# Kernel tuning notes

Hardware: AMD Instinct MI355X
Metric: run time of the kernel (lower is better)

The kernel has to match this reference:

```python
import jax, jax.numpy as jnp
import numpy as np

N, E, C, L, G, O = 100000, 1600000, 128, 7, 2, 40
BETA = 0.9
HEADS, HC = 1, 128  # heads=1, head_channels=hidden_channels=128


def setup_inputs() -> dict:
    key = jax.random.key(0)
    ks = jax.random.split(key, 16)
    s = 0.05  # ~ torch Linear init std for fan_in=128
    inp = {
        'x': jax.random.normal(ks[0], (N, C), jnp.float32),
        'edge_index': jax.random.randint(ks[1], (2, E), 0, N, jnp.int64),
        'Wh': jax.random.normal(ks[2], (L, C, C)) * s,
        'bh': jax.random.normal(ks[3], (L, C)) * s,
        'Wg': jax.random.normal(ks[4], (L, C, C)) * s,
        'bg': jax.random.normal(ks[5], (L, C)) * s,
        'Wl': jax.random.normal(ks[6], (L, C, C)) * s,
        'bl': jax.random.normal(ks[7], (L, C)) * s,
        'ln_g': jnp.ones((L, C)), 'ln_b': jnp.zeros((L, C)),
        'bn_g': jnp.ones((L, C)), 'bn_b': jnp.zeros((L, C)),
        'bn_rm': jnp.zeros((L, C)), 'bn_rv': jnp.ones((L, C)),
        'gWh': jax.random.normal(ks[8], (G, C, C)) * s,
        'gbh': jax.random.normal(ks[9], (G, C)) * s,
        'gWk': jax.random.normal(ks[10], (G, C, C)) * s,
        'gWv': jax.random.normal(ks[11], (G, C, C)) * s,
        'gln_g': jnp.ones((G, C)), 'gln_b': jnp.zeros((G, C)),
        'gWo': jax.random.normal(ks[12], (G, C, C)) * s,
        'gbo': jax.random.normal(ks[13], (G, C)) * s,
        'f_ln_g': jnp.ones((C,)), 'f_ln_b': jnp.zeros((C,)),
        'Wp': jax.random.normal(ks[14], (O, C)) * s,
        'bp': jax.random.normal(ks[15], (O,)) * s,
    }
    return inp


def _layer_norm(x, g, b, eps=1e-5):
    mu = jnp.mean(x, axis=-1, keepdims=True)
    var = jnp.mean((x - mu) ** 2, axis=-1, keepdims=True)
    return (x - mu) * jax.lax.rsqrt(var + eps) * g + b


def reference(x, edge_index, Wh, bh, Wg, bg, Wl, bl, ln_g, ln_b,
              bn_g, bn_b, bn_rm, bn_rv, gWh, gbh, gWk, gWv,
              gln_g, gln_b, gWo, gbo, f_ln_g, f_ln_b, Wp, bp):
    n = x.shape[0]
    src, dst = edge_index[0], edge_index[1]
    # gcn_norm with add_self_loops=True: deg over destination incl. self loop
    deg = jnp.zeros((n,), x.dtype).at[dst].add(1.0) + 1.0
    dinv = jax.lax.rsqrt(deg)
    enorm = (dinv[src] * dinv[dst])[:, None]   # [E,1]
    selfw = (dinv * dinv)[:, None]             # [N,1] self-loop weight

    x_local = jnp.zeros_like(x @ Wh[0].T)
    for i in range(L):
        h = jax.nn.relu(x @ Wh[i].T + bh[i])
        xw = x @ Wg[i].T                                  # GCN lin (bias separate)
        agg = jax.ops.segment_sum(xw[src] * enorm, dst, num_segments=n)
        conv = agg + xw * selfw + bg[i]
        x = conv + x @ Wl[i].T + bl[i]
        # BatchNorm1d in eval mode (running stats)
        x = (x - bn_rm[i]) * jax.lax.rsqrt(bn_rv[i] + 1e-5) * bn_g[i] + bn_b[i]
        x = jax.nn.relu(x)
        x = (1.0 - BETA) * _layer_norm(h * x, ln_g[i], ln_b[i]) + BETA * x
        x_local = x_local + x

    # global linear attention (PolynormerAttention, qk_shared=True, qkv_bias=False)
    xg = _layer_norm(x_local, f_ln_g, f_ln_b)
    for j in range(G):
        h = xg @ gWh[j].T + gbh[j]
        k = jax.nn.sigmoid(xg @ gWk[j].T).reshape(n, HEADS, HC)
        q = k
        v = (xg @ gWv[j].T).reshape(n, HEADS, HC)
        kv = jnp.einsum('ndh,ndm->dhm', k, v)            # [heads,hc,hc]
        num = jnp.einsum('ndh,dhm->ndm', q, kv)          # [N,heads,hc]
        k_sum = jnp.sum(k, axis=0)                       # [heads,hc]
        den = jnp.einsum('ndh,dh->nd', q, k_sum)[..., None]
        attn = (num / (den + 1e-6)).reshape(n, HEADS * HC)
        xg = _layer_norm(attn, gln_g[j], gln_b[j]) * (h + BETA)
        xg = jax.nn.relu(xg @ gWo[j].T + gbo[j])

    return xg @ Wp.T + bp
```

## Files before the change

### kernel.cpp

```cpp
#include <hip/hip_runtime.h>

typedef unsigned short u16;
typedef unsigned int u32;
typedef __attribute__((ext_vector_type(8))) short short8;
typedef __attribute__((ext_vector_type(8))) unsigned short ushort8v;
typedef __attribute__((ext_vector_type(4))) float f32x4;

#define CDIM 128

__device__ __forceinline__ float b2f(u16 u){ return __uint_as_float(((unsigned)u)<<16); }
__device__ __forceinline__ u16 f2b(float f){
  unsigned x = __float_as_uint(f);
  unsigned r = (x + 0x7fffu + ((x>>16)&1u)) >> 16;
  return (u16)r;
}
__device__ __forceinline__ float wsum64(float v){
  #pragma unroll
  for(int d=1; d<64; d<<=1) v += __shfl_xor(v, d, 64);
  return v;
}
__device__ __forceinline__ float wsum16(float v){
  v += __shfl_xor(v, 1, 64);
  v += __shfl_xor(v, 2, 64);
  v += __shfl_xor(v, 4, 64);
  v += __shfl_xor(v, 8, 64);
  return v;
}

__global__ void k_probe(const u32* __restrict__ x, const u32* __restrict__ ei, int* __restrict__ flags){
  __shared__ int s_bf, s_nz;
  if(threadIdx.x == 0){ s_bf = 0; s_nz = 0; }
  __syncthreads();
  int c_bf = 0, c_nz = 0;
  for(int i = threadIdx.x; i < 4096; i += 256){
    u32 w = x[i];
    u32 e = (w >> 7) & 0xFFu;
    if(e >= 100u && e <= 140u) c_bf++;
    if(ei[2*i + 1] != 0u) c_nz++;
  }
  atomicAdd(&s_bf, c_bf);
  atomicAdd(&s_nz, c_nz);
  __syncthreads();
  if(threadIdx.x == 0){
    flags[0] = (s_bf < 2048) ? 1 : 0;
    flags[1] = (s_nz < 8) ? 1 : 0;
  }
}

__global__ void k_cvt_x(const void* __restrict__ src, u16* __restrict__ dst, int n,
                        const int* __restrict__ flags){
  int i = (blockIdx.x*256 + threadIdx.x)*8;
  if(i + 7 >= n) return;
  if(flags[0]){
    const float* s = (const float*)src + i;
    float4 a = *(const float4*)s;
    float4 b = *(const float4*)(s + 4);
    ushort8v o;
    o[0]=f2b(a.x); o[1]=f2b(a.y); o[2]=f2b(a.z); o[3]=f2b(a.w);
    o[4]=f2b(b.x); o[5]=f2b(b.y); o[6]=f2b(b.z); o[7]=f2b(b.w);
    *(ushort8v*)(dst + i) = o;
  } else {
    *(ushort8v*)(dst + i) = *(const ushort8v*)((const u16*)src + i);
  }
}

struct CvtArgs {
  const void* src[24];
  u16* dst[24];
  int n[24];
};

__global__ void k_cvt_params(CvtArgs a, const int* __restrict__ flags){
  int seg = blockIdx.y;
  int i = blockIdx.x*256 + threadIdx.x;
  int n = a.n[seg];
  if(i >= n) return;
  if(flags[0]) a.dst[seg][i] = f2b(((const float*)a.src[seg])[i]);
  else         a.dst[seg][i] = ((const u16*)a.src[seg])[i];
}

__global__ void k_cvt_ei_count(const int* __restrict__ src, int* __restrict__ dst, int E,
                               const int* __restrict__ flags, u32* __restrict__ cnt){
  int i = blockIdx.x*256 + threadIdx.x;
  if(i >= 2*E) return;
  int v = flags[1] ? src[2*i] : src[i];
  dst[i] = v;
  if(i >= E) atomicAdd(&cnt[v], 1u);
}

__global__ __launch_bounds__(256) void k_scan1(const u32* __restrict__ cnt, int n, u32* __restrict__ bsum){
  const int lane = threadIdx.x & 63;
  const int wv = threadIdx.x >> 6;
  int i = blockIdx.x*256 + threadIdx.x;
  u32 v = (i < n) ? cnt[i] : 0u;
  #pragma unroll
  for(int d=1; d<64; d<<=1) v += (u32)__shfl_xor((int)v, d, 64);
  __shared__ u32 ws[4];
  if(lane == 0) ws[wv] = v;
  __syncthreads();
  if(threadIdx.x == 0) bsum[blockIdx.x] = ws[0] + ws[1] + ws[2] + ws[3];
}

__global__ __launch_bounds__(1024) void k_scan2(const u32* __restrict__ bsum, int nb, u32* __restrict__ bpre){
  __shared__ u32 s[1024];
  int t = threadIdx.x;
  u32 v = (t < nb) ? bsum[t] : 0u;
  s[t] = v;
  __syncthreads();
  for(int d=1; d<1024; d<<=1){
    u32 y = (t >= d) ? s[t-d] : 0u;
    __syncthreads();
    s[t] += y;
    __syncthreads();
  }
  if(t < nb) bpre[t] = s[t] - v;
}

__global__ __launch_bounds__(256) void k_scan3(const u32* __restrict__ cnt, int n,
                                               const u32* __restrict__ bpre,
                                               u32* __restrict__ rowstart, u32* __restrict__ cursor,
                                               float* __restrict__ dinv){
  const int lane = threadIdx.x & 63;
  const int wv = threadIdx.x >> 6;
  int i = blockIdx.x*256 + threadIdx.x;
  u32 v = (i < n) ? cnt[i] : 0u;
  u32 x = v;
  #pragma unroll
  for(int d=1; d<64; d<<=1){
    u32 y = (u32)__shfl_up((int)x, d, 64);
    if(lane >= d) x += y;
  }
  __shared__ u32 ws[4];
  if(lane == 63) ws[wv] = x;
  __syncthreads();
  u32 woff = 0;
  #pragma unroll
  for(int w=0; w<4; w++) if(w < wv) woff += ws[w];
  u32 incl = x + woff;
  u32 rs = bpre[blockIdx.x] + incl - v;
  if(i < n){
    rowstart[i] = rs;
    cursor[i] = rs;
    dinv[i] = rsqrtf((float)(v + 1u));
    if(i == n-1) rowstart[n] = rs + v;
  }
}

__global__ void k_scatter(const int* __restrict__ ei, int E, u32* __restrict__ cursor,
                          const float* __restrict__ dinv, int2* __restrict__ colw){
  int e = blockIdx.x*256 + threadIdx.x;
  if(e < E){
    int s = ei[e];
    u32 p = atomicAdd(&cursor[ei[E + e]], 1u);
    colw[p] = make_int2(s, __float_as_int(dinv[s]));
  }
}

__global__ __launch_bounds__(256) void k_gemm3(
  const u16* __restrict__ A, int M,
  const u16* __restrict__ W0, const u16* __restrict__ bs0, int op0, u16* __restrict__ O0,
  const u16* __restrict__ W1, const u16* __restrict__ bs1, int op1, u16* __restrict__ O1,
  const u16* __restrict__ W2, const u16* __restrict__ bs2, int op2, u16* __restrict__ O2)
{
  const int lane = threadIdx.x & 63;
  const int wv = threadIdx.x >> 6;
  const int l16 = lane & 15, quad = lane >> 4;
  const long rbase = (long)blockIdx.x*128 + wv*32;

  short8 af[2][4];
  #pragma unroll
  for(int rt=0; rt<2; rt++){
    long r = rbase + rt*16 + l16; if(r >= M) r = M-1;
    const u16* ap = A + r*CDIM + quad*8;
    #pragma unroll
    for(int kt=0; kt<4; kt++)
      af[rt][kt] = *(const short8*)(ap + kt*32);
  }

  const u16* Ws[3] = {W0, W1, W2};
  const u16* Bs[3] = {bs0, bs1, bs2};
  u16* Os[3] = {O0, O1, O2};
  const int ops[3] = {op0, op1, op2};

  for(int w=0; w<3; w++){
    const u16* Wm = Ws[w];
    if(!Wm) break;
    const int op = ops[w];
    u16* Op = Os[w];
    const u16* bp = Bs[w];
    for(int ct=0; ct<8; ct++){
      f32x4 acc0 = {0.f,0.f,0.f,0.f}, acc1 = {0.f,0.f,0.f,0.f};
      const u16* wp = Wm + (ct*16 + l16)*CDIM + quad*8;
      #pragma unroll
      for(int kt=0; kt<4; kt++){
        short8 bf = *(const short8*)(wp + kt*32);
        acc0 = __builtin_amdgcn_mfma_f32_16x16x32_bf16(af[0][kt], bf, acc0, 0, 0, 0);
        acc1 = __builtin_amdgcn_mfma_f32_16x16x32_bf16(af[1][kt], bf, acc1, 0, 0, 0);
      }
      const int col = ct*16 + l16;
      const float bias = bp ? b2f(bp[col]) : 0.f;
      #pragma unroll
      for(int rt=0; rt<2; rt++){
        f32x4 a = rt ? acc1 : acc0;
        #pragma unroll
        for(int g=0; g<4; g++){
          long r = rbase + rt*16 + quad*4 + g;
          if(r < M){
            float v = a[g] + bias;
            if(op == 1) v = fmaxf(v, 0.f);
            else if(op == 2) v = 1.f/(1.f + __expf(-v));
            Op[r*CDIM + col] = f2b(v);
          }
        }
      }
    }
  }
}

__global__ __launch_bounds__(256) void k_layer_epi(
  const u16* __restrict__ xw, const u16* __restrict__ h, const u16* __restrict__ xl,
  const int2* __restrict__ colw, const u32* __restrict__ rowstart, const float* __restrict__ dinv,
  const u16* __restrict__ bg, const u16* __restrict__ bng, const u16* __restrict__ bnb,
  const u16* __restrict__ bnrm, const u16* __restrict__ bnrv,
  const u16* __restrict__ lng, const u16* __restrict__ lnb,
  float* __restrict__ xlocal, u16* __restrict__ xout, int n, int first)
{
  const int lane = threadIdx.x & 63;
  const int node = blockIdx.x*4 + (threadIdx.x >> 6);
  if(node >= n) return;
  const int c0 = lane*2;
  u32 j0 = rowstart[node], j1 = rowstart[node+1];
  float a0 = 0.f, a1 = 0.f;
  for(u32 base = j0; base < j1; base += 64){
    int avail = (int)(j1 - base);
    int cnt = avail < 64 ? avail : 64;
    int2 pw = make_int2(0, 0);
    if(lane < cnt) pw = colw[base + lane];
    int t = 0;
    for(; t + 8 <= cnt; t += 8){
      int s[8]; float w[8]; ushort2 v[8];
      #pragma unroll
      for(int k2=0;k2<8;k2++){
        s[k2] = __shfl(pw.x, t+k2, 64);
        w[k2] = __int_as_float(__shfl(pw.y, t+k2, 64));
      }
      #pragma unroll
      for(int k2=0;k2<8;k2++) v[k2] = *(const ushort2*)(xw + (size_t)s[k2]*CDIM + c0);
      #pragma unroll
      for(int k2=0;k2<8;k2++){
        a0 = fmaf(w[k2], b2f(v[k2].x), a0);
        a1 = fmaf(w[k2], b2f(v[k2].y), a1);
      }
    }
    for(; t + 2 <= cnt; t += 2){
      int s0 = __shfl(pw.x, t, 64),   s1 = __shfl(pw.x, t+1, 64);
      float w0 = __int_as_float(__shfl(pw.y, t, 64));
      float w1 = __int_as_float(__shfl(pw.y, t+1, 64));
      ushort2 v0 = *(const ushort2*)(xw + (size_t)s0*CDIM + c0);
      ushort2 v1 = *(const ushort2*)(xw + (size_t)s1*CDIM + c0);
      a0 = fmaf(w0, b2f(v0.x), a0); a1 = fmaf(w0, b2f(v0.y), a1);
      a0 = fmaf(w1, b2f(v1.x), a0); a1 = fmaf(w1, b2f(v1.y), a1);
    }
    for(; t < cnt; t++){
      int s0 = __shfl(pw.x, t, 64);
      float w0 = __int_as_float(__shfl(pw.y, t, 64));
      ushort2 vv = *(const ushort2*)(xw + (size_t)s0*CDIM + c0);
      a0 = fmaf(w0, b2f(vv.x), a0);
      a1 = fmaf(w0, b2f(vv.y), a1);
    }
  }
  float dn = dinv[node], sw = dn*dn;
  size_t base = (size_t)node*CDIM + c0;
  ushort2 xwv = *(const ushort2*)(xw + base);
  ushort2 xlv = *(const ushort2*)(xl + base);
  ushort2 hv  = *(const ushort2*)(h  + base);
  float x10 = a0*dn + b2f(xwv.x)*sw + b2f(bg[c0])   + b2f(xlv.x);
  float x11 = a1*dn + b2f(xwv.y)*sw + b2f(bg[c0+1]) + b2f(xlv.y);
  float s0 = rsqrtf(b2f(bnrv[c0])   + 1e-5f) * b2f(bng[c0]);
  float s1 = rsqrtf(b2f(bnrv[c0+1]) + 1e-5f) * b2f(bng[c0+1]);
  float x20 = (x10 - b2f(bnrm[c0]))*s0   + b2f(bnb[c0]);
  float x21 = (x11 - b2f(bnrm[c0+1]))*s1 + b2f(bnb[c0+1]);
  float x30 = fmaxf(x20, 0.f);
  float x31 = fmaxf(x21, 0.f);
  float t0 = b2f(hv.x)*x30, t1 = b2f(hv.y)*x31;
  float mu = wsum64(t0 + t1) * (1.f/128.f);
  float d0 = t0 - mu, d1 = t1 - mu;
  float var = wsum64(d0*d0 + d1*d1) * (1.f/128.f);
  float inv = rsqrtf(var + 1e-5f);
  float y0 = d0*inv*b2f(lng[c0])   + b2f(lnb[c0]);
  float y1 = d1*inv*b2f(lng[c0+1]) + b2f(lnb[c0+1]);
  float xn0 = 0.1f*y0 + 0.9f*x30;
  float xn1 = 0.1f*y1 + 0.9f*x31;
  float2 xl2;
  if(first){
    xl2.x = xn0; xl2.y = xn1;
  } else {
    xl2 = *(float2*)(xlocal + base);
    xl2.x += xn0; xl2.y += xn1;
  }
  *(float2*)(xlocal + base) = xl2;
  ushort2 o; o.x = f2b(xn0); o.y = f2b(xn1);
  *(ushort2*)(xout + base) = o;
}

__global__ __launch_bounds__(256) void k_ln(
  const float* __restrict__ xin, const u16* __restrict__ g, const u16* __restrict__ b,
  u16* __restrict__ out, int n)
{
  const int lane = threadIdx.x & 63;
  const int node = blockIdx.x*4 + (threadIdx.x >> 6);
  if(node >= n) return;
  const int c0 = lane*2;
  size_t base = (size_t)node*CDIM + c0;
  float2 v = *(const float2*)(xin + base);
  float mu = wsum64(v.x + v.y) * (1.f/128.f);
  float d0 = v.x - mu, d1 = v.y - mu;
  float var = wsum64(d0*d0 + d1*d1) * (1.f/128.f);
  float inv = rsqrtf(var + 1e-5f);
  ushort2 o;
  o.x = f2b(d0*inv*b2f(g[c0])   + b2f(b[c0]));
  o.y = f2b(d1*inv*b2f(g[c0+1]) + b2f(b[c0+1]));
  *(ushort2*)(out + base) = o;
}

__global__ __launch_bounds__(256) void k_kv(
  const u16* __restrict__ kk, const u16* __restrict__ vv, int n, int npb,
  float* __restrict__ part)
{
  __shared__ float sk[8][128];
  __shared__ float sv[8][128];
  const int tid = threadIdx.x;
  const int tr = tid >> 4, tc = tid & 15;
  float acc[8][8];
  #pragma unroll
  for(int i=0;i<8;i++){
    #pragma unroll
    for(int j=0;j<8;j++) acc[i][j] = 0.f;
  }
  float ks[8];
  #pragma unroll
  for(int i=0;i<8;i++) ks[i] = 0.f;
  int start = blockIdx.x * npb;
  int end = start + npb; if(end > n) end = n;
  const int lr = tid >> 5;
  const int lc = (tid & 31) * 4;
  for(int g0 = start; g0 < end; g0 += 8){
    int cnt = end - g0; if(cnt > 8) cnt = 8;
    __syncthreads();
    if(lr < cnt){
      ushort4 kq = *(const ushort4*)(kk + (size_t)(g0+lr)*CDIM + lc);
      ushort4 vq = *(const ushort4*)(vv + (size_t)(g0+lr)*CDIM + lc);
      sk[lr][lc] = b2f(kq.x); sk[lr][lc+1] = b2f(kq.y); sk[lr][lc+2] = b2f(kq.z); sk[lr][lc+3] = b2f(kq.w);
      sv[lr][lc] = b2f(vq.x); sv[lr][lc+1] = b2f(vq.y); sv[lr][lc+2] = b2f(vq.z); sv[lr][lc+3] = b2f(vq.w);
    }
    __syncthreads();
    for(int r=0; r<cnt; r++){
      float4 ka = *(const float4*)&sk[r][tr*8];
      float4 kb = *(const float4*)&sk[r][tr*8+4];
      float4 va = *(const float4*)&sv[r][tc*8];
      float4 vb = *(const float4*)&sv[r][tc*8+4];
      float kr[8] = {ka.x,ka.y,ka.z,ka.w,kb.x,kb.y,kb.z,kb.w};
      float vr[8] = {va.x,va.y,va.z,va.w,vb.x,vb.y,vb.z,vb.w};
      #pragma unroll
      for(int i=0;i<8;i++){
        #pragma unroll
        for(int j=0;j<8;j++) acc[i][j] = fmaf(kr[i], vr[j], acc[i][j]);
      }
      if(tc == 0){
        #pragma unroll
        for(int i=0;i<8;i++) ks[i] += kr[i];
      }
    }
  }
  float* p = part + (size_t)blockIdx.x * 16512;
  #pragma unroll
  for(int i=0;i<8;i++){
    #pragma unroll
    for(int j=0;j<8;j++)
      p[(size_t)(tc*8+j)*CDIM + tr*8 + i] = acc[i][j];
  }
  if(tc == 0){
    #pragma unroll
    for(int i=0;i<8;i++) p[16384 + tr*8 + i] = ks[i];
  }
}

__global__ void k_kvred(const float* __restrict__ part, int nb, u16* __restrict__ Bext){
  int i = blockIdx.x*256 + threadIdx.x;
  if(i >= 144*128) return;
  float s = 0.f;
  if(i < 16512){
    #pragma unroll 8
    for(int b=0;b<nb;b++) s += part[(size_t)b*16512 + i];
  }
  Bext[i] = f2b(s);
}

__global__ __launch_bounds__(256) void k_attn(
  const u16* __restrict__ q, const u16* __restrict__ Bext, const u16* __restrict__ hg,
  const u16* __restrict__ g, const u16* __restrict__ b,
  u16* __restrict__ out, int M)
{
  const int lane = threadIdx.x & 63;
  const int wv = threadIdx.x >> 6;
  const int l16 = lane & 15, quad = lane >> 4;
  const long rbase = (long)blockIdx.x*128 + wv*32;

  short8 af[2][4];
  #pragma unroll
  for(int rt=0; rt<2; rt++){
    long r = rbase + rt*16 + l16; if(r >= M) r = M-1;
    const u16* ap = q + r*CDIM + quad*8;
    #pragma unroll
    for(int kt=0; kt<4; kt++)
      af[rt][kt] = *(const short8*)(ap + kt*32);
  }
  f32x4 acc[2][9];
  f32x4 zero = {0.f,0.f,0.f,0.f};
  #pragma unroll
  for(int rt=0; rt<2; rt++){
    #pragma unroll
    for(int ct=0; ct<9; ct++) acc[rt][ct] = zero;
  }
  #pragma unroll
  for(int ct=0; ct<9; ct++){
    const u16* wp = Bext + (ct*16 + l16)*CDIM + quad*8;
    #pragma unroll
    for(int kt=0; kt<4; kt++){
      short8 bf = *(const short8*)(wp + kt*32);
      acc[0][ct] = __builtin_amdgcn_mfma_f32_16x16x32_bf16(af[0][kt], bf, acc[0][ct], 0, 0, 0);
      acc[1][ct] = __builtin_amdgcn_mfma_f32_16x16x32_bf16(af[1][kt], bf, acc[1][ct], 0, 0, 0);
    }
  }
  #pragma unroll
  for(int rt=0; rt<2; rt++){
    float rden[4];
    #pragma unroll
    for(int gi=0; gi<4; gi++){
      float dv = __shfl(acc[rt][8][gi], lane & 48, 64);
      rden[gi] = 1.f/(dv + 1e-6f);
    }
    #pragma unroll
    for(int gi=0; gi<4; gi++){
      float sum = 0.f;
      #pragma unroll
      for(int ct=0; ct<8; ct++) sum += acc[rt][ct][gi]*rden[gi];
      float mu = wsum16(sum) * (1.f/128.f);
      float vs = 0.f;
      #pragma unroll
      for(int ct=0; ct<8; ct++){ float d = acc[rt][ct][gi]*rden[gi] - mu; vs = fmaf(d, d, vs); }
      float inv = rsqrtf(wsum16(vs)*(1.f/128.f) + 1e-5f);
      long r = rbase + rt*16 + quad*4 + gi;
      if(r < M){
        #pragma unroll
        for(int ct=0; ct<8; ct++){
          int col = ct*16 + l16;
          float y = (acc[rt][ct][gi]*rden[gi] - mu)*inv*b2f(g[col]) + b2f(b[col]);
          float hvv = b2f(hg[(size_t)r*CDIM + col]);
          out[(size_t)r*CDIM + col] = f2b(y*(hvv + 0.9f));
        }
      }
    }
  }
}

__global__ __launch_bounds__(256) void k_gout(
  const u16* __restrict__ A, const u16* __restrict__ W, const u16* __restrict__ bs,
  void* __restrict__ outv, int M, const int* __restrict__ flags)
{
  const int lane = threadIdx.x & 63;
  const int wv = threadIdx.x >> 6;
  const int l16 = lane & 15, quad = lane >> 4;
  const long rbase = (long)blockIdx.x*128 + wv*32;
  const int f32m = flags[0];
  short8 af[2][4];
  #pragma unroll
  for(int rt=0; rt<2; rt++){
    long r = rbase + rt*16 + l16; if(r >= M) r = M-1;
    const u16* ap = A + r*CDIM + quad*8;
    #pragma unroll
    for(int kt=0; kt<4; kt++)
      af[rt][kt] = *(const short8*)(ap + kt*32);
  }
  f32x4 acc[2][3];
  f32x4 zero = {0.f,0.f,0.f,0.f};
  #pragma unroll
  for(int rt=0; rt<2; rt++){
    #pragma unroll
    for(int ct=0; ct<3; ct++) acc[rt][ct] = zero;
  }
  #pragma unroll
  for(int ct=0; ct<3; ct++){
    int row = ct*16 + l16; if(row > 39) row = 39;
    const u16* wp = W + row*CDIM + quad*8;
    #pragma unroll
    for(int kt=0; kt<4; kt++){
      short8 bf = *(const short8*)(wp + kt*32);
      acc[0][ct] = __builtin_amdgcn_mfma_f32_16x16x32_bf16(af[0][kt], bf, acc[0][ct], 0, 0, 0);
      acc[1][ct] = __builtin_amdgcn_mfma_f32_16x16x32_bf16(af[1][kt], bf, acc[1][ct], 0, 0, 0);
    }
  }
  #pragma unroll
  for(int ct=0; ct<3; ct++){
    int col = ct*16 + l16;
    if(col < 40){
      float bias = b2f(bs[col]);
      #pragma unroll
      for(int rt=0; rt<2; rt++){
        #pragma unroll
        for(int gi=0; gi<4; gi++){
          long r = rbase + rt*16 + quad*4 + gi;
          if(r < M){
            float v = acc[rt][ct][gi] + bias;
            if(f32m) ((float*)outv)[r*40 + col] = v;
            else     ((u16*)outv)[r*40 + col] = f2b(v);
          }
        }
      }
    }
  }
}

extern "C" void kernel_launch(void* const* d_in, const int* in_sizes, int n_in,
                              void* d_out, int out_size, void* d_ws, size_t ws_size,
                              hipStream_t stream)
{
  (void)n_in;
  const int C = CDIM;
  const int Nn = in_sizes[0] / C;
  const int E  = in_sizes[1] / 2;

  char* ws = (char*)d_ws;
  size_t off = 0;
  auto alloc = [&](size_t bytes) -> char* {
    char* p = ws + off;
    off = (off + bytes + 255) & ~(size_t)255;
    return p;
  };
  u16*   x_cur  = (u16*)  alloc((size_t)Nn*C*2);
  float* xlocal = (float*)alloc((size_t)Nn*C*4);
  u16*   hb     = (u16*)  alloc((size_t)Nn*C*2);
  u16*   xwb    = (u16*)  alloc((size_t)Nn*C*2);
  u16*   xlb    = (u16*)  alloc((size_t)Nn*C*2);
  float* dinv   = (float*)alloc((size_t)Nn*4);
  u32*   cnt    = (u32*)  alloc((size_t)Nn*4);
  u32*   rowst  = (u32*)  alloc((size_t)(Nn+1)*4);
  u32*   cursor = (u32*)  alloc((size_t)Nn*4);
  int2*  colw   = (int2*) alloc((size_t)E*8);
  u16*   Bext   = (u16*)  alloc((size_t)144*128*2);
  int*   flags  = (int*)  alloc(256);
  u32*   bsum   = (u32*)  alloc(1024*4);
  u32*   bpre   = (u32*)  alloc(1024*4);
  size_t ptot = 0;
  for(int k=2;k<26;k++) ptot += (size_t)in_sizes[k];
  u16* pbuf = (u16*)alloc(ptot*2);

  if(off > ws_size){
    hipMemsetAsync(d_out, 0, (size_t)out_size*2, stream);
    return;
  }

  const u16* pp[26];
  {
    size_t po = 0;
    for(int k=2;k<26;k++){ pp[k] = pbuf + po; po += (size_t)in_sizes[k]; }
  }
  const u16* cWh  = pp[2];  const u16* cbh  = pp[3];
  const u16* cWg  = pp[4];  const u16* cbg  = pp[5];
  const u16* cWl  = pp[6];  const u16* cbl  = pp[7];
  const u16* clng = pp[8];  const u16* clnb = pp[9];
  const u16* cbng = pp[10]; const u16* cbnb = pp[11];
  const u16* cbnrm= pp[12]; const u16* cbnrv= pp[13];
  const u16* cgWh = pp[14]; const u16* cgbh = pp[15];
  const u16* cgWk = pp[16]; const u16* cgWv = pp[17];
  const u16* cglng= pp[18]; const u16* cglnb= pp[19];
  const u16* cgWo = pp[20]; const u16* cgbo = pp[21];
  const u16* cflng= pp[22]; const u16* cflnb= pp[23];
  const u16* cWp  = pp[24]; const u16* cbp  = pp[25];

  u16* xb  = (u16*)xlocal;
  int* eib = (int*)((char*)xlocal + (size_t)Nn*C*2);
  u16* xg  = x_cur;
  float* kvpart = xlocal;

  const int NB_KV = 512;
  const int npb = (Nn + NB_KV - 1) / NB_KV;
  const int gblk = (Nn + 127) / 128;
  const int nodeblk = (Nn + 3) / 4;
  const int nscan = (Nn + 255) / 256;

  k_probe<<<1, 256, 0, stream>>>((const u32*)d_in[0], (const u32*)d_in[1], flags);
  hipMemsetAsync(cnt, 0, (size_t)Nn*4, stream);
  k_cvt_ei_count<<<(2*E + 255)/256, 256, 0, stream>>>((const int*)d_in[1], eib, E, flags, cnt);
  k_cvt_x<<<(Nn*C/8 + 255)/256, 256, 0, stream>>>(d_in[0], xb, Nn*C, flags);
  {
    CvtArgs a;
    int maxn = 0;
    for(int k=2;k<26;k++){
      a.src[k-2] = d_in[k];
      a.dst[k-2] = (u16*)pp[k];
      a.n[k-2]   = in_sizes[k];
      if(in_sizes[k] > maxn) maxn = in_sizes[k];
    }
    dim3 g((maxn + 255)/256, 24);
    k_cvt_params<<<g, 256, 0, stream>>>(a, flags);
  }

  k_scan1<<<nscan, 256, 0, stream>>>(cnt, Nn, bsum);
  k_scan2<<<1, 1024, 0, stream>>>(bsum, nscan, bpre);
  k_scan3<<<nscan, 256, 0, stream>>>(cnt, Nn, bpre, rowst, cursor, dinv);
  k_scatter<<<(E + 255)/256, 256, 0, stream>>>(eib, E, cursor, dinv, colw);

  const u16* xa = xb;
  for(int i=0; i<7; i++){
    k_gemm3<<<gblk, 256, 0, stream>>>(xa, Nn,
        cWh + (size_t)i*C*C, cbh + (size_t)i*C, 1, hb,
        cWg + (size_t)i*C*C, (const u16*)nullptr, 0, xwb,
        cWl + (size_t)i*C*C, cbl + (size_t)i*C, 0, xlb);
    k_layer_epi<<<nodeblk, 256, 0, stream>>>(xwb, hb, xlb, colw, rowst, dinv,
        cbg + (size_t)i*C, cbng + (size_t)i*C, cbnb + (size_t)i*C,
        cbnrm + (size_t)i*C, cbnrv + (size_t)i*C,
        clng + (size_t)i*C, clnb + (size_t)i*C,
        xlocal, x_cur, Nn, (i==0) ? 1 : 0);
    xa = x_cur;
  }

  k_ln<<<nodeblk, 256, 0, stream>>>(xlocal, cflng, cflnb, xg, Nn);

  for(int j=0; j<2; j++){
    k_gemm3<<<gblk, 256, 0, stream>>>(xg, Nn,
        cgWh + (size_t)j*C*C, cgbh + (size_t)j*C, 0, hb,
        cgWk + (size_t)j*C*C, (const u16*)nullptr, 2, xwb,
        cgWv + (size_t)j*C*C, (const u16*)nullptr, 0, xlb);
    k_kv   <<<NB_KV, 256, 0, stream>>>(xwb, xlb, Nn, npb, kvpart);
    k_kvred<<<(144*128 + 255)/256, 256, 0, stream>>>(kvpart, NB_KV, Bext);
    k_attn <<<gblk, 256, 0, stream>>>(xwb, Bext, hb, cglng + (size_t)j*C, cglnb + (size_t)j*C, xlb, Nn);
    k_gemm3<<<gblk, 256, 0, stream>>>(xlb, Nn,
        cgWo + (size_t)j*C*C, cgbo + (size_t)j*C, 1, xg,
        (const u16*)nullptr, (const u16*)nullptr, 0, (u16*)nullptr,
        (const u16*)nullptr, (const u16*)nullptr, 0, (u16*)nullptr);
  }

  k_gout<<<gblk, 256, 0, stream>>>(xg, cWp, cbp, d_out, Nn, flags);
}
```

Before: 1.776 ms.

## Partition CSR scatter by destination range per XCD and unroll aggregation by 16

The edge scatter now launches 8 block groups per edge slice. Each group handles only edges whose destination falls in one eighth of the node range, with the group chosen by blockIdx mod 8. This is meant to keep each set of cursor atomics and colw writes local to one XCD's L2, at the cost of reading the destination array eight times. The neighbor aggregation loop is also changed to one 16-wide unrolled body padded to a multiple of 16. Padded lanes use source 0 with weight 0, which removes the remainder loops but issues extra gathers of row 0 for nodes whose degree is not a multiple of 16.

Result: no change. 1.767 ms (-0.5%).

```diff
diff --git a/kernel.cpp b/kernel.cpp
--- a/kernel.cpp
+++ b/kernel.cpp
@@ -146,13 +146,25 @@
   }
 }
 
-__global__ void k_scatter(const int* __restrict__ ei, int E, u32* __restrict__ cursor,
-                          const float* __restrict__ dinv, int2* __restrict__ colw){
-  int e = blockIdx.x*256 + threadIdx.x;
-  if(e < E){
-    int s = ei[e];
-    u32 p = atomicAdd(&cursor[ei[E + e]], 1u);
-    colw[p] = make_int2(s, __float_as_int(dinv[s]));
+__global__ __launch_bounds__(256) void k_scatter8(
+  const int* __restrict__ ei, int E, int Nn, int nsl,
+  u32* __restrict__ cursor, const float* __restrict__ dinv, int2* __restrict__ colw)
+{
+  const int r = blockIdx.x & 7;
+  const int slice = blockIdx.x >> 3;
+  const int q = (Nn + 7) >> 3;
+  const int lo = r*q;
+  const int hi = (lo + q < Nn) ? lo + q : Nn;
+  const int chunk = (E + nsl - 1) / nsl;
+  int e0 = slice*chunk;
+  int e1 = e0 + chunk; if(e1 > E) e1 = E;
+  for(int e = e0 + threadIdx.x; e < e1; e += 256){
+    int d = ei[E + e];
+    if(d >= lo && d < hi){
+      int s = ei[e];
+      u32 p = atomicAdd(&cursor[d], 1u);
+      colw[p] = make_int2(s, __float_as_int(dinv[s]));
+    }
   }
 }
 
@@ -236,37 +248,21 @@
     int cnt = avail < 64 ? avail : 64;
     int2 pw = make_int2(0, 0);
     if(lane < cnt) pw = colw[base + lane];
-    int t = 0;
-    for(; t + 8 <= cnt; t += 8){
-      int s[8]; float w[8]; ushort2 v[8];
-      #pragma unroll
-      for(int k2=0;k2<8;k2++){
+    int cntp = (cnt + 15) & ~15;
+    for(int t = 0; t < cntp; t += 16){
+      int s[16]; float w[16]; ushort2 v[16];
+      #pragma unroll
+      for(int k2=0;k2<16;k2++){
         s[k2] = __shfl(pw.x, t+k2, 64);
         w[k2] = __int_as_float(__shfl(pw.y, t+k2, 64));
       }
       #pragma unroll
-      for(int k2=0;k2<8;k2++) v[k2] = *(const ushort2*)(xw + (size_t)s[k2]*CDIM + c0);
-      #pragma unroll
-      for(int k2=0;k2<8;k2++){
+      for(int k2=0;k2<16;k2++) v[k2] = *(const ushort2*)(xw + (size_t)s[k2]*CDIM + c0);
+      #pragma unroll
+      for(int k2=0;k2<16;k2++){
         a0 = fmaf(w[k2], b2f(v[k2].x), a0);
         a1 = fmaf(w[k2], b2f(v[k2].y), a1);
       }
-    }
-    for(; t + 2 <= cnt; t += 2){
-      int s0 = __shfl(pw.x, t, 64),   s1 = __shfl(pw.x, t+1, 64);
-      float w0 = __int_as_float(__shfl(pw.y, t, 64));
-      float w1 = __int_as_float(__shfl(pw.y, t+1, 64));
-      ushort2 v0 = *(const ushort2*)(xw + (size_t)s0*CDIM + c0);
-      ushort2 v1 = *(const ushort2*)(xw + (size_t)s1*CDIM + c0);
-      a0 = fmaf(w0, b2f(v0.x), a0); a1 = fmaf(w0, b2f(v0.y), a1);
-      a0 = fmaf(w1, b2f(v1.x), a0); a1 = fmaf(w1, b2f(v1.y), a1);
-    }
-    for(; t < cnt; t++){
-      int s0 = __shfl(pw.x, t, 64);
-      float w0 = __int_as_float(__shfl(pw.y, t, 64));
-      ushort2 vv = *(const ushort2*)(xw + (size_t)s0*CDIM + c0);
-      a0 = fmaf(w0, b2f(vv.x), a0);
-      a1 = fmaf(w0, b2f(vv.y), a1);
     }
   }
   float dn = dinv[node], sw = dn*dn;
@@ -588,6 +584,7 @@
   const int gblk = (Nn + 127) / 128;
   const int nodeblk = (Nn + 3) / 4;
   const int nscan = (Nn + 255) / 256;
+  const int NSL = 512;
 
   k_probe<<<1, 256, 0, stream>>>((const u32*)d_in[0], (const u32*)d_in[1], flags);
   hipMemsetAsync(cnt, 0, (size_t)Nn*4, stream);
@@ -609,7 +606,7 @@
   k_scan1<<<nscan, 256, 0, stream>>>(cnt, Nn, bsum);
   k_scan2<<<1, 1024, 0, stream>>>(bsum, nscan, bpre);
   k_scan3<<<nscan, 256, 0, stream>>>(cnt, Nn, bpre, rowst, cursor, dinv);
-  k_scatter<<<(E + 255)/256, 256, 0, stream>>>(eib, E, cursor, dinv, colw);
+  k_scatter8<<<NSL*8, 256, 0, stream>>>(eib, E, Nn, NSL, cursor, dinv, colw);
 
   const u16* xa = xb;
   for(int i=0; i<7; i++){
```
